# Kernel tuning notes

Measured on AMD Instinct MI355X. Metric: run time of the kernel, lower is better.

Reference implementation:

```python
import jax, jax.numpy as jnp
import numpy as np

WS = 8
NH = 6
LF_DIM = 64
HF_DIM = 192
HEAD_DIM = HF_DIM // NH


def _rpb_index(ws):
    # static numpy computation of the relative-position index, (N, N) int
    coords = np.stack(np.meshgrid(np.arange(ws), np.arange(ws), indexing='ij')).reshape(2, -1)
    rel = coords[:, :, None] - coords[:, None, :]          # (2, N, N)
    rel = rel.transpose(1, 2, 0).astype(np.int64)          # (N, N, 2)
    rel[..., 0] += ws - 1
    rel[..., 1] += ws - 1
    rel[..., 0] *= 2 * ws - 1
    return rel.sum(-1)                                     # (N, N)

_RPB_IDX = _rpb_index(WS)


def _layernorm(x, g, b, eps=1e-5):
    mu = jnp.mean(x, axis=-1, keepdims=True)
    var = jnp.mean(jnp.square(x - mu), axis=-1, keepdims=True)
    return (x - mu) * jax.lax.rsqrt(var + eps) * g + b


def _window_partition(x, ws):
    # (B, C, H, W) -> (B*nH*nW, ws*ws, C)
    B, C, H, W = x.shape
    x = x.reshape(B, C, H // ws, ws, W // ws, ws)
    x = x.transpose(0, 2, 4, 3, 5, 1)                      # B nH nW ws ws C
    return x.reshape(-1, ws * ws, C)


def _window_reverse(wins, ws, H, W):
    # (B*nH*nW, ws*ws, C) -> (B, C, H, W)
    nH, nW = H // ws, W // ws
    B = wins.shape[0] // (nH * nW)
    C = wins.shape[-1]
    x = wins.reshape(B, nH, nW, ws, ws, C)
    x = x.transpose(0, 5, 1, 3, 2, 4)                      # B C nH ws nW ws
    return x.reshape(B, C, H, W)


def setup_inputs() -> dict:
    key = jax.random.key(0)
    ks = jax.random.split(key, 16)
    B, H, W = 4, 256, 256
    s = 0.02
    return {
        'y_lf': jax.random.normal(ks[0], (B, LF_DIM, H, W), jnp.float32),
        'y_hf': jax.random.normal(ks[1], (B, HF_DIM, H, W), jnp.float32),
        'norm_lf_g': jnp.ones((LF_DIM,), jnp.float32),
        'norm_lf_b': jnp.zeros((LF_DIM,), jnp.float32),
        'norm_hf_g': jnp.ones((HF_DIM,), jnp.float32),
        'norm_hf_b': jnp.zeros((HF_DIM,), jnp.float32),
        'Wq': jax.random.normal(ks[2], (LF_DIM, HF_DIM), jnp.float32) * s,
        'bq': jnp.zeros((HF_DIM,), jnp.float32),
        'Wk': jax.random.normal(ks[3], (HF_DIM, HF_DIM), jnp.float32) * s,
        'bk': jnp.zeros((HF_DIM,), jnp.float32),
        'Wv': jax.random.normal(ks[4], (HF_DIM, HF_DIM), jnp.float32) * s,
        'bv': jnp.zeros((HF_DIM,), jnp.float32),
        'Wo': jax.random.normal(ks[5], (HF_DIM, HF_DIM), jnp.float32) * s,
        'bo': jnp.zeros((HF_DIM,), jnp.float32),
        'rpb_table': jax.random.normal(ks[6], ((2 * WS - 1) ** 2, NH), jnp.float32) * s,
    }


def reference(y_lf, y_hf, norm_lf_g, norm_lf_b, norm_hf_g, norm_hf_b,
              Wq, bq, Wk, bk, Wv, bv, Wo, bo, rpb_table):
    B, _, H, W = y_lf.shape
    ws, N = WS, WS * WS
    # H, W chosen divisible by ws so the reflect-pad in the original is a no-op
    lf_w = _window_partition(y_lf, ws)                     # (bw, N, C_lf)
    hf_w = _window_partition(y_hf, ws)                     # (bw, N, C_hf)
    hf_residual = hf_w
    lf_n = _layernorm(lf_w, norm_lf_g, norm_lf_b)
    hf_n = _layernorm(hf_w, norm_hf_g, norm_hf_b)
    bw = lf_w.shape[0]
    Q = (lf_n @ Wq + bq).reshape(bw, N, NH, HEAD_DIM).transpose(0, 2, 1, 3)
    K = (hf_n @ Wk + bk).reshape(bw, N, NH, HEAD_DIM).transpose(0, 2, 1, 3)
    V = (hf_n @ Wv + bv).reshape(bw, N, NH, HEAD_DIM).transpose(0, 2, 1, 3)
    scale = HEAD_DIM ** -0.5
    attn = jnp.einsum('bhnd,bhmd->bhnm', Q, K) * scale     # (bw, h, N, N)
    bias = rpb_table[_RPB_IDX.reshape(-1)].reshape(N, N, NH).transpose(2, 0, 1)
    attn = jax.nn.softmax(attn + bias[None], axis=-1)
    out = jnp.einsum('bhnm,bhmd->bhnd', attn, V)
    out = out.transpose(0, 2, 1, 3).reshape(bw, N, HF_DIM)
    out = out @ Wo + bo + hf_residual
    return _window_reverse(out, ws, H, W)                  # (B, C_hf, H, W)
```

## Files before the change

### kernel.cpp

```cpp
#include <hip/hip_runtime.h>
#include <cstdint>
#include <cstddef>

#define DEVI __device__ __forceinline__

typedef __bf16 bf16x8 __attribute__((ext_vector_type(8)));
typedef float  floatx4 __attribute__((ext_vector_type(4)));

constexpr int NHEAD = 6;
constexpr int CLF = 64, CHF = 192;
constexpr int IMG = 256;
constexpr int HW  = IMG * IMG;

constexpr int OFF_WKV = 0;
constexpr int OFF_WO  = 24576;
constexpr int OFF_K   = 36864;
constexpr int OFF_VT  = 45056;
constexpr int OFF_PW  = 49152;
constexpr int OFF_RPB = 58368;
constexpr int SMEM_BYTES = 61072;
constexpr int P_PW = 72;

constexpr int LOFF_LF  = 25600;
constexpr int LOFF_RED = 34816;
constexpr int P_HFL = 200, P_LFL = 72;
constexpr int P_WQ = 72;

DEVI unsigned short f2b(float f) {
  unsigned u = __float_as_uint(f);
  u += 0x7fffu + ((u >> 16) & 1u);
  return (unsigned short)(u >> 16);
}
DEVI float b2f(unsigned short s) { return __uint_as_float(((unsigned)s) << 16); }

DEVI floatx4 mfma_bf16(bf16x8 a, bf16x8 b, floatx4 c) {
  return __builtin_amdgcn_mfma_f32_16x16x32_bf16(a, b, c, 0, 0, 0);
}

DEVI int swz8(int row, int off) { return off ^ ((row & 7) << 3); }
DEVI int swz4(int row, int off) { return off ^ ((row & 3) << 3); }

__global__ void wca_prep(const float* __restrict__ Wq, const float* __restrict__ Wk,
                         const float* __restrict__ Wv, const float* __restrict__ Wo,
                         unsigned short* __restrict__ wT) {
  int i = blockIdx.x * 256 + threadIdx.x;
  if (i < 12288) {
    int n = i >> 6, k = i & 63;
    wT[i] = f2b(Wq[k * 192 + n]);
  } else if (i < 49152) {
    int j = i - 12288, n = j / 192, k = j - n * 192;
    wT[i] = f2b(Wk[k * 192 + n]);
  } else if (i < 86016) {
    int j = i - 49152, n = j / 192, k = j - n * 192;
    wT[i] = f2b(Wv[k * 192 + n]);
  } else {
    int j = i - 86016, n = j / 192, k = j - n * 192;
    wT[i] = f2b(Wo[k * 192 + n]);
  }
}

__global__ __launch_bounds__(256, 2) void wca_main(
    const float* __restrict__ ylf, const float* __restrict__ yhf,
    const float* __restrict__ glf, const float* __restrict__ blf,
    const float* __restrict__ ghf, const float* __restrict__ bhf,
    const float* __restrict__ bq,  const float* __restrict__ bk,
    const float* __restrict__ bv,  const float* __restrict__ bo,
    const float* __restrict__ rpb, const unsigned short* __restrict__ wT,
    float* __restrict__ out) {
  __shared__ __align__(16) char smem[SMEM_BYTES];
  unsigned short* s_wkv = (unsigned short*)(smem + OFF_WKV);
  unsigned short* s_wo  = (unsigned short*)(smem + OFF_WO);
  unsigned short* s_k   = (unsigned short*)(smem + OFF_K);
  unsigned short* s_vt  = (unsigned short*)(smem + OFF_VT);
  unsigned short* s_rpb = (unsigned short*)(smem + OFF_RPB);
  unsigned short* s_hfL = (unsigned short*)(smem);
  unsigned short* s_lfL = (unsigned short*)(smem + LOFF_LF);
  float* s_red = (float*)(smem + LOFF_RED);
  unsigned short* s_wq = (unsigned short*)(smem);

  const int tid  = threadIdx.x;
  const int lane = tid & 63;
  const int wv   = tid >> 6;
  const int quad = lane >> 4;
  const int l16  = lane & 15;
  unsigned short* s_pw = (unsigned short*)(smem + OFF_PW) + wv * 16 * P_PW;

  const int g   = blockIdx.x;
  const int wid = ((g & 7) << 9) | (g >> 3);
  const int b   = wid >> 10;
  const int wy  = (wid >> 5) & 31;
  const int wx  = wid & 31;
  const int h0  = wy << 3, w0 = wx << 3;

  const int t_own = tid & 63;
  const int cg    = tid >> 6;
  const int ty    = t_own >> 3, tx = t_own & 7;

  float lfv[16], hfv[48];
  float ls = 0.f, l2 = 0.f, hs = 0.f, h2 = 0.f;
  {
    const float* p = ylf + ((size_t)(b * CLF + cg * 16) * IMG + (h0 + ty)) * IMG + (w0 + tx);
#pragma unroll
    for (int k = 0; k < 16; k++) {
      float v = p[(size_t)k * HW];
      lfv[k] = v; ls += v; l2 += v * v;
    }
  }
  {
    const float* p = yhf + ((size_t)(b * CHF + cg * 48) * IMG + (h0 + ty)) * IMG + (w0 + tx);
#pragma unroll
    for (int k = 0; k < 48; k++) {
      float v = p[(size_t)k * HW];
      hfv[k] = v; hs += v; h2 += v * v;
    }
  }
  s_red[0 * 256 + (cg << 6) + t_own] = ls;
  s_red[1 * 256 + (cg << 6) + t_own] = l2;
  s_red[2 * 256 + (cg << 6) + t_own] = hs;
  s_red[3 * 256 + (cg << 6) + t_own] = h2;
  __syncthreads();
  float su = 0.f, sq = 0.f, hu = 0.f, hq = 0.f;
#pragma unroll
  for (int gg = 0; gg < 4; gg++) {
    su += s_red[0 * 256 + (gg << 6) + t_own];
    sq += s_red[1 * 256 + (gg << 6) + t_own];
    hu += s_red[2 * 256 + (gg << 6) + t_own];
    hq += s_red[3 * 256 + (gg << 6) + t_own];
  }
  const float mu_lf = su * (1.f / 64.f);
  const float rs_lf = rsqrtf(sq * (1.f / 64.f) - mu_lf * mu_lf + 1e-5f);
  const float mu_hf = hu * (1.f / 192.f);
  const float rs_hf = rsqrtf(hq * (1.f / 192.f) - mu_hf * mu_hf + 1e-5f);

#pragma unroll
  for (int j = 0; j < 4; j++) {
    uint64_t w = 0;
#pragma unroll
    for (int m = 0; m < 4; m++) {
      int c = cg * 16 + j * 4 + m;
      float v = (lfv[j * 4 + m] - mu_lf) * rs_lf * glf[c] + blf[c];
      w |= (uint64_t)f2b(v) << (16 * m);
    }
    *(uint64_t*)(s_lfL + t_own * P_LFL + cg * 16 + j * 4) = w;
  }
#pragma unroll
  for (int j = 0; j < 12; j++) {
    uint64_t w = 0;
#pragma unroll
    for (int m = 0; m < 4; m++) {
      int c = cg * 48 + j * 4 + m;
      float v = (hfv[j * 4 + m] - mu_hf) * rs_hf * ghf[c] + bhf[c];
      w |= (uint64_t)f2b(v) << (16 * m);
    }
    *(uint64_t*)(s_hfL + t_own * P_HFL + cg * 48 + j * 4) = w;
  }
  __syncthreads();

  const int myrow = wv * 16 + l16;
  bf16x8 lfr0 = *(const bf16x8*)(s_lfL + myrow * P_LFL + quad * 8);
  bf16x8 lfr1 = *(const bf16x8*)(s_lfL + myrow * P_LFL + 32 + quad * 8);
  bf16x8 hfr[6];
#pragma unroll
  for (int ks = 0; ks < 6; ks++)
    hfr[ks] = *(const bf16x8*)(s_hfL + myrow * P_HFL + ks * 32 + quad * 8);
  __syncthreads();

  const unsigned short* wqT = wT;
  const unsigned short* wkT = wT + 12288;
  const unsigned short* wvT = wT + 49152;
  const unsigned short* woT = wT + 86016;

#pragma unroll
  for (int i = 0; i < 6; i++) {
    int p = i * 256 + tid;
    int n = p >> 3, sub = p & 7;
    *(uint4*)(s_wq + n * P_WQ + sub * 8) = *(const uint4*)(wqT + n * 64 + sub * 8);
  }
  for (int i = tid; i < 225 * NHEAD; i += 256) s_rpb[i] = f2b(rpb[i]);
  __syncthreads();

  const int rowbase = wv * 16 + quad * 4;

  bf16x8 aq[NHEAD];
#pragma unroll
  for (int h = 0; h < NHEAD; h++) {
#pragma unroll
    for (int nt = 0; nt < 2; nt++) {
      const int n = h * 32 + nt * 16 + l16;
      floatx4 acc = {0.f, 0.f, 0.f, 0.f};
      acc = mfma_bf16(lfr0, *(const bf16x8*)(s_wq + n * P_WQ + quad * 8), acc);
      acc = mfma_bf16(lfr1, *(const bf16x8*)(s_wq + n * P_WQ + 32 + quad * 8), acc);
      const float bqv = bq[n];
#pragma unroll
      for (int r = 0; r < 4; r++)
        s_pw[(quad * 4 + r) * P_PW + nt * 16 + l16] = f2b(acc[r] + bqv);
    }
    aq[h] = *(const bf16x8*)(s_pw + l16 * P_PW + quad * 8);
  }
  __syncthreads();

  auto stageKV = [&](int h) {
    const unsigned short* sk = wkT + h * 6144;
    const unsigned short* sv = wvT + h * 6144;
#pragma unroll
    for (int i = 0; i < 3; i++) {
      int p = i * 256 + tid;
      int nl = p / 24, sub = p - nl * 24;
      *(uint4*)(s_wkv + nl * 192 + swz8(nl, sub * 8)) =
          *(const uint4*)(sk + nl * 192 + sub * 8);
      *(uint4*)(s_wkv + (32 + nl) * 192 + swz8(32 + nl, sub * 8)) =
          *(const uint4*)(sv + nl * 192 + sub * 8);
    }
  };

  stageKV(0);
  __syncthreads();

  floatx4 oa[12];
  const floatx4 zero = {0.f, 0.f, 0.f, 0.f};
#pragma unroll
  for (int ct = 0; ct < 12; ct++) oa[ct] = zero;

#pragma unroll
  for (int h = 0; h < NHEAD; h++) {
#pragma unroll
    for (int nt = 0; nt < 2; nt++) {
      const int n = h * 32 + nt * 16 + l16;
      const int nl = nt * 16 + l16;
      floatx4 a0 = zero, a1 = zero;
#pragma unroll
      for (int ks = 0; ks < 3; ks++) {
        a0 = mfma_bf16(hfr[ks],
            *(const bf16x8*)(s_wkv + nl * 192 + swz8(nl, ks * 32 + quad * 8)), a0);
        a1 = mfma_bf16(hfr[ks + 3],
            *(const bf16x8*)(s_wkv + nl * 192 + swz8(nl, (ks + 3) * 32 + quad * 8)), a1);
      }
      floatx4 acc = a0 + a1;
      const float bkv = bk[n];
#pragma unroll
      for (int r = 0; r < 4; r++)
        s_k[(rowbase + r) * 64 + swz8(rowbase + r, nt * 16 + l16)] = f2b(acc[r] + bkv);
    }
#pragma unroll
    for (int nt = 0; nt < 2; nt++) {
      const int n = h * 32 + nt * 16 + l16;
      const int nl = nt * 16 + l16;
      floatx4 a0 = zero, a1 = zero;
#pragma unroll
      for (int ks = 0; ks < 3; ks++) {
        a0 = mfma_bf16(hfr[ks],
            *(const bf16x8*)(s_wkv + (32 + nl) * 192 + swz8(32 + nl, ks * 32 + quad * 8)), a0);
        a1 = mfma_bf16(hfr[ks + 3],
            *(const bf16x8*)(s_wkv + (32 + nl) * 192 + swz8(32 + nl, (ks + 3) * 32 + quad * 8)), a1);
      }
      floatx4 acc = a0 + a1;
      const float bvv = bv[n];
#pragma unroll
      for (int r = 0; r < 4; r++)
        s_vt[nl * 64 + swz8(nl, rowbase + r)] = f2b(acc[r] + bvv);
    }
    __syncthreads();

#pragma unroll
    for (int i = 0; i < 3; i++) {
      int p = i * 256 + tid;
      int n = p >> 2, sub = p & 3;
      *(uint4*)(s_wo + n * 32 + swz4(n, sub * 8)) =
          *(const uint4*)(woT + n * 192 + h * 32 + sub * 8);
    }
    if (h + 1 < NHEAD) stageKV(h + 1);

    float sv[4][4];
#pragma unroll
    for (int ct = 0; ct < 4; ct++) {
      const int kr = ct * 16 + l16;
      bf16x8 kb = *(const bf16x8*)(s_k + kr * 64 + swz8(kr, quad * 8));
      floatx4 acc = zero;
      acc = mfma_bf16(aq[h], kb, acc);
#pragma unroll
      for (int r = 0; r < 4; r++) {
        int row = rowbase + r, col = kr;
        int dy = (row >> 3) - (col >> 3) + 7;
        int dx = (row & 7) - (col & 7) + 7;
        sv[ct][r] = acc[r] * 0.17677669529663688f + b2f(s_rpb[(dy * 15 + dx) * NHEAD + h]);
      }
    }
#pragma unroll
    for (int r = 0; r < 4; r++) {
      const float L2E = 1.4426950408889634f;
      float e0 = exp2f(sv[0][r] * L2E);
      float e1 = exp2f(sv[1][r] * L2E);
      float e2 = exp2f(sv[2][r] * L2E);
      float e3 = exp2f(sv[3][r] * L2E);
      float s = e0 + e1 + e2 + e3;
      s += __shfl_xor(s, 1);
      s += __shfl_xor(s, 2);
      s += __shfl_xor(s, 4);
      s += __shfl_xor(s, 8);
      float inv = 1.f / s;
      sv[0][r] = e0 * inv; sv[1][r] = e1 * inv; sv[2][r] = e2 * inv; sv[3][r] = e3 * inv;
    }
#pragma unroll
    for (int ct = 0; ct < 4; ct++)
#pragma unroll
      for (int r = 0; r < 4; r++)
        s_pw[(quad * 4 + r) * P_PW + ct * 16 + l16] = f2b(sv[ct][r]);

    floatx4 pv0 = zero, pv1 = zero;
#pragma unroll
    for (int ks = 0; ks < 2; ks++) {
      bf16x8 pa = *(const bf16x8*)(s_pw + l16 * P_PW + ks * 32 + quad * 8);
      pv0 = mfma_bf16(pa, *(const bf16x8*)(s_vt + l16 * 64 + swz8(l16, ks * 32 + quad * 8)), pv0);
      pv1 = mfma_bf16(pa, *(const bf16x8*)(s_vt + (16 + l16) * 64 + swz8(16 + l16, ks * 32 + quad * 8)), pv1);
    }
#pragma unroll
    for (int r = 0; r < 4; r++) {
      s_pw[(quad * 4 + r) * P_PW + l16]      = f2b(pv0[r]);
      s_pw[(quad * 4 + r) * P_PW + 16 + l16] = f2b(pv1[r]);
    }
    bf16x8 aoh = *(const bf16x8*)(s_pw + l16 * P_PW + quad * 8);
    __syncthreads();

#pragma unroll
    for (int ct = 0; ct < 12; ct++) {
      bf16x8 bb = *(const bf16x8*)(s_wo + (ct * 16 + l16) * 32 + swz4(ct * 16 + l16, quad * 8));
      oa[ct] = mfma_bf16(aoh, bb, oa[ct]);
    }
  }
  __syncthreads();

  unsigned short* s_ostg = (unsigned short*)(smem);
#pragma unroll
  for (int ct = 0; ct < 12; ct++) {
    const int col = ct * 16 + l16;
    const float bov = bo[col];
#pragma unroll
    for (int r = 0; r < 4; r++)
      s_ostg[(rowbase + r) * 200 + col] = f2b(oa[ct][r] + bov);
  }
  __syncthreads();

#pragma unroll
  for (int k = 0; k < 12; k++) {
    int chunk = k * 256 + tid;
    int c   = chunk >> 4;
    int sub = chunk & 15;
    int yy  = sub >> 1;
    int x4  = (sub & 1) << 2;
    int t0  = (yy << 3) + x4;
    size_t gidx = ((size_t)(b * CHF + c) * IMG + (h0 + yy)) * IMG + w0 + x4;
    float4 res = *(const float4*)(yhf + gidx);
    float4 v;
    v.x = b2f(s_ostg[(t0 + 0) * 200 + c]) + res.x;
    v.y = b2f(s_ostg[(t0 + 1) * 200 + c]) + res.y;
    v.z = b2f(s_ostg[(t0 + 2) * 200 + c]) + res.z;
    v.w = b2f(s_ostg[(t0 + 3) * 200 + c]) + res.w;
    *(float4*)(out + gidx) = v;
  }
}

extern "C" void kernel_launch(void* const* d_in, const int* in_sizes, int n_in,
                              void* d_out, int out_size, void* d_ws, size_t ws_size,
                              hipStream_t stream) {
  const float* ylf = (const float*)d_in[0];
  const float* yhf = (const float*)d_in[1];
  const float* glf = (const float*)d_in[2];
  const float* blf = (const float*)d_in[3];
  const float* ghf = (const float*)d_in[4];
  const float* bhf = (const float*)d_in[5];
  const float* Wq  = (const float*)d_in[6];
  const float* bq  = (const float*)d_in[7];
  const float* Wk  = (const float*)d_in[8];
  const float* bk  = (const float*)d_in[9];
  const float* Wv  = (const float*)d_in[10];
  const float* bv  = (const float*)d_in[11];
  const float* Wo  = (const float*)d_in[12];
  const float* bo  = (const float*)d_in[13];
  const float* rpb = (const float*)d_in[14];
  unsigned short* wT = (unsigned short*)d_ws;

  wca_prep<<<480, 256, 0, stream>>>(Wq, Wk, Wv, Wo, wT);
  wca_main<<<4096, 256, 0, stream>>>(ylf, yhf, glf, blf, ghf, bhf,
                                     bq, bk, bv, bo, rpb, wT, (float*)d_out);
}
```

Measured before the change: 627.0 us.

## Defer output projection to epilogue, keep per-head outputs in registers, raise occupancy

The per-head Wo slice staging and the 12 fp32 output accumulators are removed from the head loop. Each head's attention output is instead kept as a bf16 fragment in registers, and the output projection runs after the loop in three 64-column passes that stage Wo through the freed K/V weight region. This shrinks LDS use to about 50KB and the accumulator register footprint, so launch bounds are raised to 3 blocks per CU. The cost is an extra staging-and-sync phase at the end and less overlap of the Wo work with attention.

```diff
diff --git a/kernel.cpp b/kernel.cpp
--- a/kernel.cpp
+++ b/kernel.cpp
@@ -13,12 +13,12 @@
 constexpr int HW  = IMG * IMG;
 
 constexpr int OFF_WKV = 0;
-constexpr int OFF_WO  = 24576;
-constexpr int OFF_K   = 36864;
-constexpr int OFF_VT  = 45056;
-constexpr int OFF_PW  = 49152;
-constexpr int OFF_RPB = 58368;
-constexpr int SMEM_BYTES = 61072;
+constexpr int OFF_K   = 24576;
+constexpr int OFF_VT  = 32768;
+constexpr int OFF_PW  = 36864;
+constexpr int OFF_RPB = 46080;
+constexpr int OFF_EPO = 24576;
+constexpr int SMEM_BYTES = 50176;
 constexpr int P_PW = 72;
 
 constexpr int LOFF_LF  = 25600;
@@ -38,7 +38,6 @@
 }
 
 DEVI int swz8(int row, int off) { return off ^ ((row & 7) << 3); }
-DEVI int swz4(int row, int off) { return off ^ ((row & 3) << 3); }
 
 __global__ void wca_prep(const float* __restrict__ Wq, const float* __restrict__ Wk,
                          const float* __restrict__ Wv, const float* __restrict__ Wo,
@@ -59,7 +58,7 @@
   }
 }
 
-__global__ __launch_bounds__(256, 2) void wca_main(
+__global__ __launch_bounds__(256, 3) void wca_main(
     const float* __restrict__ ylf, const float* __restrict__ yhf,
     const float* __restrict__ glf, const float* __restrict__ blf,
     const float* __restrict__ ghf, const float* __restrict__ bhf,
@@ -69,14 +68,15 @@
     float* __restrict__ out) {
   __shared__ __align__(16) char smem[SMEM_BYTES];
   unsigned short* s_wkv = (unsigned short*)(smem + OFF_WKV);
-  unsigned short* s_wo  = (unsigned short*)(smem + OFF_WO);
   unsigned short* s_k   = (unsigned short*)(smem + OFF_K);
   unsigned short* s_vt  = (unsigned short*)(smem + OFF_VT);
   unsigned short* s_rpb = (unsigned short*)(smem + OFF_RPB);
   unsigned short* s_hfL = (unsigned short*)(smem);
   unsigned short* s_lfL = (unsigned short*)(smem + LOFF_LF);
   float* s_red = (float*)(smem + LOFF_RED);
-  unsigned short* s_wq = (unsigned short*)(smem);
+  unsigned short* s_wq  = (unsigned short*)(smem);
+  unsigned short* s_ep  = (unsigned short*)(smem);
+  unsigned short* s_os  = (unsigned short*)(smem + OFF_EPO);
 
   const int tid  = threadIdx.x;
   const int lane = tid & 63;
@@ -216,10 +216,8 @@
   stageKV(0);
   __syncthreads();
 
-  floatx4 oa[12];
   const floatx4 zero = {0.f, 0.f, 0.f, 0.f};
-#pragma unroll
-  for (int ct = 0; ct < 12; ct++) oa[ct] = zero;
+  bf16x8 aob[NHEAD];
 
 #pragma unroll
   for (int h = 0; h < NHEAD; h++) {
@@ -261,13 +259,6 @@
     }
     __syncthreads();
 
-#pragma unroll
-    for (int i = 0; i < 3; i++) {
-      int p = i * 256 + tid;
-      int n = p >> 2, sub = p & 3;
-      *(uint4*)(s_wo + n * 32 + swz4(n, sub * 8)) =
-          *(const uint4*)(woT + n * 192 + h * 32 + sub * 8);
-    }
     if (h + 1 < NHEAD) stageKV(h + 1);
 
     float sv[4][4];
@@ -318,27 +309,36 @@
       s_pw[(quad * 4 + r) * P_PW + l16]      = f2b(pv0[r]);
       s_pw[(quad * 4 + r) * P_PW + 16 + l16] = f2b(pv1[r]);
     }
-    bf16x8 aoh = *(const bf16x8*)(s_pw + l16 * P_PW + quad * 8);
+    aob[h] = *(const bf16x8*)(s_pw + l16 * P_PW + quad * 8);
     __syncthreads();
-
-#pragma unroll
-    for (int ct = 0; ct < 12; ct++) {
-      bf16x8 bb = *(const bf16x8*)(s_wo + (ct * 16 + l16) * 32 + swz4(ct * 16 + l16, quad * 8));
-      oa[ct] = mfma_bf16(aoh, bb, oa[ct]);
-    }
-  }
-  __syncthreads();
-
-  unsigned short* s_ostg = (unsigned short*)(smem);
-#pragma unroll
-  for (int ct = 0; ct < 12; ct++) {
-    const int col = ct * 16 + l16;
-    const float bov = bo[col];
-#pragma unroll
-    for (int r = 0; r < 4; r++)
-      s_ostg[(rowbase + r) * 200 + col] = f2b(oa[ct][r] + bov);
-  }
-  __syncthreads();
+  }
+
+#pragma unroll
+  for (int t = 0; t < 3; t++) {
+#pragma unroll
+    for (int i = 0; i < 6; i++) {
+      int p = i * 256 + tid;
+      int nl = p / 24, sub = p - nl * 24;
+      *(uint4*)(s_ep + nl * 192 + swz8(nl, sub * 8)) =
+          *(const uint4*)(woT + (t * 64 + nl) * 192 + sub * 8);
+    }
+    __syncthreads();
+#pragma unroll
+    for (int c4 = 0; c4 < 4; c4++) {
+      const int nl = c4 * 16 + l16;
+      floatx4 acc = zero;
+#pragma unroll
+      for (int ks = 0; ks < 6; ks++)
+        acc = mfma_bf16(aob[ks],
+            *(const bf16x8*)(s_ep + nl * 192 + swz8(nl, ks * 32 + quad * 8)), acc);
+      const int col = t * 64 + c4 * 16 + l16;
+      const float bov = bo[col];
+#pragma unroll
+      for (int r = 0; r < 4; r++)
+        s_os[(rowbase + r) * 200 + col] = f2b(acc[r] + bov);
+    }
+    __syncthreads();
+  }
 
 #pragma unroll
   for (int k = 0; k < 12; k++) {
@@ -351,10 +351,10 @@
     size_t gidx = ((size_t)(b * CHF + c) * IMG + (h0 + yy)) * IMG + w0 + x4;
     float4 res = *(const float4*)(yhf + gidx);
     float4 v;
-    v.x = b2f(s_ostg[(t0 + 0) * 200 + c]) + res.x;
-    v.y = b2f(s_ostg[(t0 + 1) * 200 + c]) + res.y;
-    v.z = b2f(s_ostg[(t0 + 2) * 200 + c]) + res.z;
-    v.w = b2f(s_ostg[(t0 + 3) * 200 + c]) + res.w;
+    v.x = b2f(s_os[(t0 + 0) * 200 + c]) + res.x;
+    v.y = b2f(s_os[(t0 + 1) * 200 + c]) + res.y;
+    v.z = b2f(s_os[(t0 + 2) * 200 + c]) + res.z;
+    v.w = b2f(s_os[(t0 + 3) * 200 + c]) + res.w;
     *(float4*)(out + gidx) = v;
   }
 }
```

Measured after the change: 654.4 us. +4.4%, slower.
